# Optimization experiments

Hardware: AMD Instinct MI355X
Metric: run time of the kernel (lower is better)

Reference implementation:

```python
import jax, jax.numpy as jnp
import numpy as np

N = 20000
E = 320000
R1 = 8        # num_rels (layer 1)
R2 = 256      # layer-2 num_rels == out_size (faithful to original positional-arg bug)
B = 8         # num_bases
D = 256       # hid_size == out_size
TIME_DIM = 2880
POI_DIM = 12
ROAD_DIM = 32


def relconv(h, src, dst, etype, coeff, bases, loop_w, bias):
    """DGL RelGraphConv with basis regularizer, sum aggregation, self-loop, bias.
    W_r = sum_b coeff[r,b] * bases[b]; msg_e = h[src_e] @ W_{etype_e}; agg = scatter-add to dst.
    Implemented memory-efficiently: project nodes into basis space once [B,N,D],
    then scan over the B bases (small fixed loop) for the gather/scale/scatter.
    """
    tb = jnp.einsum('nd,bdo->bno', h, bases)          # [B, N, D]
    c = coeff[etype]                                   # [E, B] per-edge basis coeffs

    def body(agg, xs):
        tb_b, c_b = xs                                 # [N,D], [E]
        msg = c_b[:, None] * tb_b[src]                 # [E, D]
        return agg + jax.ops.segment_sum(msg, dst, num_segments=N), None

    agg0 = jnp.zeros((N, bases.shape[-1]), h.dtype)
    agg, _ = jax.lax.scan(body, agg0, (tb, c.T))
    return agg + h @ loop_w + bias


def rgcn2(feat, src, dst, etype, c1, v1, l1, b1, c2, v2, l2, b2):
    h = relconv(feat, src, dst, etype, c1, v1, l1, b1)
    h = jax.nn.relu(h)  # dropout p=0.0 -> identity
    h = relconv(h, src, dst, etype, c2, v2, l2, b2)
    return h


def setup_inputs() -> dict:
    key = jax.random.key(0)
    ks = iter(jax.random.split(key, 48))
    f32 = jnp.float32

    def nrm(shape, std=0.02):
        return (jax.random.normal(next(ks), shape, dtype=f32) * std)

    inp = {
        'poi_distribution': jax.random.uniform(next(ks), (N, POI_DIM), dtype=f32),
        'time_distribution': jax.random.normal(next(ks), (N, TIME_DIM), dtype=f32),
        'road_feature': jax.random.normal(next(ks), (N, ROAD_DIM), dtype=f32),
        # input projections (torch Linear: stored here as [in,out])
        'W_poi': nrm((POI_DIM, 64)), 'b_poi': jnp.zeros((64,), f32),
        'W_time': nrm((TIME_DIM, 128)), 'b_time': jnp.zeros((128,), f32),
        'W_road': nrm((ROAD_DIM, 64)), 'b_road': jnp.zeros((64,), f32),
        # adj R-GCN layer params: coeff [R,B], bases [B,D,D], loop [D,D], bias [D]
        'a_coeff1': nrm((R1, B), 0.3), 'a_bases1': nrm((B, D, D)),
        'a_loop1': nrm((D, D)), 'a_bias1': jnp.zeros((D,), f32),
        'a_coeff2': nrm((R2, B), 0.3), 'a_bases2': nrm((B, D, D)),
        'a_loop2': nrm((D, D)), 'a_bias2': jnp.zeros((D,), f32),
        # no_adj R-GCN layer params
        'n_coeff1': nrm((R1, B), 0.3), 'n_bases1': nrm((B, D, D)),
        'n_loop1': nrm((D, D)), 'n_bias1': jnp.zeros((D,), f32),
        'n_coeff2': nrm((R2, B), 0.3), 'n_bases2': nrm((B, D, D)),
        'n_loop2': nrm((D, D)), 'n_bias2': jnp.zeros((D,), f32),
        # fusion
        'W_fuse': nrm((D, D)), 'b_fuse': jnp.zeros((D,), f32),
        'W_fuse_kg': nrm((D, D)), 'b_fuse_kg': jnp.zeros((D,), f32),
        # graphs (edge lists + relation types)
        'adj_src': jax.random.randint(next(ks), (E,), 0, N, dtype=jnp.int32),
        'adj_dst': jax.random.randint(next(ks), (E,), 0, N, dtype=jnp.int32),
        'adj_type': jax.random.randint(next(ks), (E,), 0, R1, dtype=jnp.int32),
        'no_adj_src': jax.random.randint(next(ks), (E,), 0, N, dtype=jnp.int32),
        'no_adj_dst': jax.random.randint(next(ks), (E,), 0, N, dtype=jnp.int32),
        'no_adj_type': jax.random.randint(next(ks), (E,), 0, R1, dtype=jnp.int32),
    }
    return inp


def reference(poi_distribution, time_distribution, road_feature,
              W_poi, b_poi, W_time, b_time, W_road, b_road,
              a_coeff1, a_bases1, a_loop1, a_bias1,
              a_coeff2, a_bases2, a_loop2, a_bias2,
              n_coeff1, n_bases1, n_loop1, n_bias1,
              n_coeff2, n_bases2, n_loop2, n_bias2,
              W_fuse, b_fuse, W_fuse_kg, b_fuse_kg,
              adj_src, adj_dst, adj_type,
              no_adj_src, no_adj_dst, no_adj_type):
    poi_feat = poi_distribution @ W_poi + b_poi       # [N, 64]
    time_feat = time_distribution @ W_time + b_time   # [N, 128]
    road_feat = road_feature @ W_road + b_road        # [N, 64]
    feat = jnp.concatenate([poi_feat, time_feat, road_feat], axis=1)  # [N, 256]

    adj_emb = rgcn2(feat, adj_src, adj_dst, adj_type,
                    a_coeff1, a_bases1, a_loop1, a_bias1,
                    a_coeff2, a_bases2, a_loop2, a_bias2)
    no_adj_emb = rgcn2(feat, no_adj_src, no_adj_dst, no_adj_type,
                       n_coeff1, n_bases1, n_loop1, n_bias1,
                       n_coeff2, n_bases2, n_loop2, n_bias2)

    fused = (adj_emb @ W_fuse + b_fuse) + (no_adj_emb @ W_fuse_kg + b_fuse_kg)
    return jax.nn.gelu(fused, approximate=False)      # torch nn.GELU is exact erf
```

## Files before the change

kernel.cpp:

```cpp
#include <hip/hip_runtime.h>
#include <math.h>

typedef unsigned short ushort_t;
typedef __bf16 bf16x8 __attribute__((ext_vector_type(8)));
typedef float  f32x4  __attribute__((ext_vector_type(4)));

constexpr int NN = 20000;
constexpr int EE = 320000;
constexpr int NC = 2304;
constexpr int TD = 2880;

__device__ __forceinline__ float b2f(ushort_t u) {
    return __uint_as_float(((unsigned int)u) << 16);
}
__device__ __forceinline__ ushort_t f2b(float f) {
    unsigned int u = __float_as_uint(f);
    u += 0x7fffu + ((u >> 16) & 1u);
    return (ushort_t)(u >> 16);
}
__device__ __forceinline__ float ldf(const void* p, size_t i, int f32m) {
    return f32m ? ((const float*)p)[i] : b2f(((const ushort_t*)p)[i]);
}
__device__ __forceinline__ void gl2lds16(const ushort_t* g, ushort_t* l) {
    __builtin_amdgcn_global_load_lds(
        (const __attribute__((address_space(1))) void*)g,
        (__attribute__((address_space(3))) void*)l, 16, 0, 0);
}

__device__ __forceinline__ void mfma_step(const ushort_t* As, const ushort_t* Bs,
                                          f32x4 (&acc)[4][4],
                                          int wm, int wn, int quad, int l16)
{
    bf16x8 afr[4], bfr[4];
#pragma unroll
    for (int mi = 0; mi < 4; mi++)
        afr[mi] = *(const bf16x8*)(As + (wm * 64 + mi * 16 + l16) * 32 + quad * 8);
#pragma unroll
    for (int ni = 0; ni < 4; ni++)
        bfr[ni] = *(const bf16x8*)(Bs + (wn * 64 + ni * 16 + l16) * 32 + quad * 8);
#pragma unroll
    for (int mi = 0; mi < 4; mi++)
#pragma unroll
        for (int ni = 0; ni < 4; ni++)
            acc[mi][ni] = __builtin_amdgcn_mfma_f32_16x16x32_bf16(
                afr[mi], bfr[ni], acc[mi][ni], 0, 0, 0);
}

__global__ void k_detect(const void* timeD, int* flags)
{
    __shared__ float mx[256];
    int t = threadIdx.x;
    float m = 0.f;
    for (int i = t; i < 1024; i += 256) {
        float v = fabsf(b2f(((const ushort_t*)timeD)[i]));
        if (!(v < 1e30f)) v = 1e30f;
        m = fmaxf(m, v);
    }
    mx[t] = m;
    __syncthreads();
    if (t == 0) {
        float mm = 0.f;
        for (int i = 0; i < 256; i++) mm = fmaxf(mm, mx[i]);
        flags[0] = (mm > 1e4f) ? 1 : 0;
        flags[1] = 0;
    }
}

__global__ void k_cvt16(const void* __restrict__ in, ushort_t* __restrict__ out,
                        int n, const int* __restrict__ mf)
{
    int f32m = mf[0];
    int i = blockIdx.x * 256 + threadIdx.x;
    if (i < n) out[i] = f32m ? f2b(((const float*)in)[i]) : ((const ushort_t*)in)[i];
}

__global__ __launch_bounds__(256) void gemm_bt(
    const ushort_t* __restrict__ A, int lda,
    const ushort_t* __restrict__ Bt, int ldb,
    void* __restrict__ C, int ldc, int col0, const int* __restrict__ of,
    const ushort_t* __restrict__ bias,
    int M, int Ncols, int K, int act)
{
    __shared__ ushort_t As[128 * 32];
    __shared__ ushort_t Bs[128 * 32];

    const int f32o = of[0];
    const int t    = threadIdx.x;
    const int wave = t >> 6, lane = t & 63;
    const int wm   = wave >> 1, wn = wave & 1;
    const int quad = lane >> 4, l16 = lane & 15;
    const int m0   = blockIdx.x * 128, n0 = blockIdx.y * 128;

    f32x4 acc[4][4];
#pragma unroll
    for (int i = 0; i < 4; i++)
#pragma unroll
        for (int j = 0; j < 4; j++) acc[i][j] = (f32x4){0.f, 0.f, 0.f, 0.f};

    for (int k0 = 0; k0 < K; k0 += 32) {
#pragma unroll
        for (int j = 0; j < 2; j++) {
            int c   = (wave * 2 + j) * 64 + lane;
            int row = c >> 2, kc = c & 3;
            ushort_t* ldsbase_a = As + (wave * 2 + j) * 512;
            ushort_t* ldsbase_b = Bs + (wave * 2 + j) * 512;
            gl2lds16(A  + (size_t)(m0 + row) * lda + k0 + kc * 8, ldsbase_a);
            gl2lds16(Bt + (size_t)(n0 + row) * ldb + k0 + kc * 8, ldsbase_b);
        }
        __syncthreads();
        mfma_step(As, Bs, acc, wm, wn, quad, l16);
        __syncthreads();
    }

#pragma unroll
    for (int mi = 0; mi < 4; mi++) {
#pragma unroll
        for (int r = 0; r < 4; r++) {
            int row = m0 + wm * 64 + mi * 16 + quad * 4 + r;
            if (row >= M) continue;
#pragma unroll
            for (int ni = 0; ni < 4; ni++) {
                int col = n0 + wn * 64 + ni * 16 + l16;
                float v = acc[mi][ni][r];
                if (bias) v += b2f(bias[col]);
                if (act == 1) v = fmaxf(v, 0.f);
                else if (act == 2) v = 0.5f * v * (1.f + erff(v * 0.70710678118654752f));
                size_t idx = (size_t)row * ldc + col0 + col;
                if (f32o) ((float*)C)[idx] = v;
                else      ((ushort_t*)C)[idx] = f2b(v);
            }
        }
    }
}

__global__ __launch_bounds__(256) void gemm_splitk(
    const void* __restrict__ A, int lda, const int* __restrict__ af,
    const ushort_t* __restrict__ Bt, int ldb,
    float* __restrict__ part, int M, int K, int KC)
{
    __shared__ ushort_t As[128 * 32];
    __shared__ ushort_t Bs[128 * 32];

    const int f32a = af[0];
    const int t    = threadIdx.x;
    const int wave = t >> 6, lane = t & 63;
    const int wm   = wave >> 1, wn = wave & 1;
    const int quad = lane >> 4, l16 = lane & 15;
    const int m0   = blockIdx.x * 128;
    const int kbeg = blockIdx.y * KC;
    const int kend = (kbeg + KC < K) ? kbeg + KC : K;

    f32x4 acc[4][4];
#pragma unroll
    for (int i = 0; i < 4; i++)
#pragma unroll
        for (int j = 0; j < 4; j++) acc[i][j] = (f32x4){0.f, 0.f, 0.f, 0.f};

    if (!f32a && (m0 + 128 <= M)) {
        const ushort_t* Ab = (const ushort_t*)A;
        for (int k0 = kbeg; k0 < kend; k0 += 32) {
#pragma unroll
            for (int j = 0; j < 2; j++) {
                int c   = (wave * 2 + j) * 64 + lane;
                int row = c >> 2, kc = c & 3;
                gl2lds16(Ab + (size_t)(m0 + row) * lda + k0 + kc * 8,
                         As + (wave * 2 + j) * 512);
                gl2lds16(Bt + (size_t)row * ldb + k0 + kc * 8,
                         Bs + (wave * 2 + j) * 512);
            }
            __syncthreads();
            mfma_step(As, Bs, acc, wm, wn, quad, l16);
            __syncthreads();
        }
    } else {
        for (int k0 = kbeg; k0 < kend; k0 += 32) {
#pragma unroll
            for (int i = 0; i < 2; i++) {
                int c = t + i * 256;
                int row = c >> 2, kc = c & 3;
                uint4 av = make_uint4(0, 0, 0, 0);
                int gr = m0 + row;
                if (gr < M) {
                    size_t base = (size_t)gr * lda + k0 + kc * 8;
                    if (f32a) {
                        const float* Af = (const float*)A + base;
                        float4 lo = *(const float4*)Af;
                        float4 hi = *(const float4*)(Af + 4);
                        av.x = (unsigned)f2b(lo.x) | ((unsigned)f2b(lo.y) << 16);
                        av.y = (unsigned)f2b(lo.z) | ((unsigned)f2b(lo.w) << 16);
                        av.z = (unsigned)f2b(hi.x) | ((unsigned)f2b(hi.y) << 16);
                        av.w = (unsigned)f2b(hi.z) | ((unsigned)f2b(hi.w) << 16);
                    } else {
                        av = *(const uint4*)((const ushort_t*)A + base);
                    }
                }
                *(uint4*)(As + row * 32 + kc * 8) = av;
                uint4 bv = *(const uint4*)(Bt + (size_t)row * ldb + k0 + kc * 8);
                *(uint4*)(Bs + row * 32 + kc * 8) = bv;
            }
            __syncthreads();
            mfma_step(As, Bs, acc, wm, wn, quad, l16);
            __syncthreads();
        }
    }

    float* dst = part + (size_t)blockIdx.y * ((size_t)M * 128);
#pragma unroll
    for (int mi = 0; mi < 4; mi++) {
#pragma unroll
        for (int r = 0; r < 4; r++) {
            int row = m0 + wm * 64 + mi * 16 + quad * 4 + r;
            if (row >= M) continue;
#pragma unroll
            for (int ni = 0; ni < 4; ni++) {
                int col = wn * 64 + ni * 16 + l16;
                dst[(size_t)row * 128 + col] = acc[mi][ni][r];
            }
        }
    }
}

__global__ void k_bias_time(const float* __restrict__ part, int nsplit,
                            const ushort_t* __restrict__ bt,
                            ushort_t* __restrict__ feat)
{
    int n = blockIdx.x, o = threadIdx.x;
    float a = b2f(bt[o]);
    for (int s = 0; s < nsplit; ++s)
        a += part[(size_t)s * NN * 128 + (size_t)n * 128 + o];
    feat[(size_t)n * 256 + 64 + o] = f2b(a);
}

__global__ void k_build_wcat(const void* __restrict__ coeff,
                             const void* __restrict__ bases,
                             const void* __restrict__ loopw,
                             ushort_t* __restrict__ Wt, const int* __restrict__ mf)
{
    int f32m = mf[0];
    int r = blockIdx.x >> 8, k = blockIdx.x & 255, o = threadIdx.x;
    float acc;
    if (r == 8) {
        acc = ldf(loopw, k * 256 + o, f32m);
    } else {
        acc = 0.f;
#pragma unroll
        for (int b = 0; b < 8; b++)
            acc += ldf(coeff, r * 8 + b, f32m) * ldf(bases, ((size_t)b * 256 + k) * 256 + o, f32m);
    }
    Wt[((size_t)(r * 256 + o)) * 256 + k] = f2b(acc);
}

__global__ void k_transpose(const void* __restrict__ in, ushort_t* __restrict__ out,
                            int rows, int cols, const int* __restrict__ mf)
{
    int f32m = mf[0];
    int k = blockIdx.x, o = threadIdx.x;
    out[(size_t)o * rows + k] = f2b(ldf(in, (size_t)k * cols + o, f32m));
}

__global__ void k_build_wfuse(const void* __restrict__ Wf, const void* __restrict__ Wfk,
                              const void* __restrict__ bf, const void* __restrict__ bfk,
                              ushort_t* __restrict__ Wt, ushort_t* __restrict__ bias_cat,
                              const int* __restrict__ mf)
{
    int f32m = mf[0];
    int k = blockIdx.x, o = threadIdx.x;
    float v = (k < 256) ? ldf(Wf, k * 256 + o, f32m) : ldf(Wfk, (k - 256) * 256 + o, f32m);
    Wt[(size_t)o * 512 + k] = f2b(v);
    if (k == 0) bias_cat[o] = f2b(ldf(bf, o, f32m) + ldf(bfk, o, f32m));
}

__global__ void k_inproj(const void* __restrict__ poi, const void* __restrict__ Wp,
                         const void* __restrict__ bp,
                         const void* __restrict__ road, const void* __restrict__ Wr,
                         const void* __restrict__ br,
                         ushort_t* __restrict__ feat, const int* __restrict__ mf)
{
    int f32m = mf[0];
    int n = blockIdx.x, t = threadIdx.x;
    if (t < 64) {
        float a = ldf(bp, t, f32m);
#pragma unroll
        for (int k = 0; k < 12; k++)
            a += ldf(poi, (size_t)n * 12 + k, f32m) * ldf(Wp, k * 64 + t, f32m);
        feat[(size_t)n * 256 + t] = f2b(a);
    } else {
        int o = t - 64;
        float a = ldf(br, o, f32m);
#pragma unroll
        for (int k = 0; k < 32; k++)
            a += ldf(road, (size_t)n * 32 + k, f32m) * ldf(Wr, k * 64 + o, f32m);
        feat[(size_t)n * 256 + 192 + o] = f2b(a);
    }
}

__global__ void k_zero(int* __restrict__ p, int n)
{
    int i = blockIdx.x * 256 + threadIdx.x;
    if (i < n) p[i] = 0;
}
__global__ void k_count(const int* __restrict__ dst, int* __restrict__ deg, int e)
{
    int i = blockIdx.x * 256 + threadIdx.x;
    if (i < e) atomicAdd(&deg[dst[i]], 1);
}
__global__ void k_scan1(const int* __restrict__ deg, int* __restrict__ partial,
                        int* __restrict__ bsum, int n)
{
    int t = threadIdx.x, b = blockIdx.x;
    int i = b * 256 + t;
    int v = (i < n) ? deg[i] : 0;
    int lane = t & 63, w = t >> 6;
    int x = v;
#pragma unroll
    for (int d = 1; d < 64; d <<= 1) {
        int y = __shfl_up(x, d);
        if (lane >= d) x += y;
    }
    __shared__ int wt[4];
    if (lane == 63) wt[w] = x;
    __syncthreads();
    int woff = 0;
    for (int j = 0; j < 4; j++) if (j < w) woff += wt[j];
    int incl = x + woff;
    if (i < n) partial[i] = incl - v;
    if (t == 255) bsum[b] = incl;
}
__global__ void k_scan2(const int* __restrict__ bsum, int* __restrict__ boff, int nb)
{
    int t = threadIdx.x;
    int v = (t < nb) ? bsum[t] : 0;
    int lane = t & 63, w = t >> 6;
    int x = v;
#pragma unroll
    for (int d = 1; d < 64; d <<= 1) {
        int y = __shfl_up(x, d);
        if (lane >= d) x += y;
    }
    __shared__ int wt[4];
    if (lane == 63) wt[w] = x;
    __syncthreads();
    int woff = 0;
    for (int j = 0; j < 4; j++) if (j < w) woff += wt[j];
    boff[t] = (x + woff) - v;
}
__global__ void k_scan3(const int* __restrict__ boff, int* __restrict__ rs,
                        int* __restrict__ cur, int n)
{
    int i = blockIdx.x * 256 + threadIdx.x;
    if (i < n) {
        int v = rs[i] + boff[blockIdx.x];
        rs[i] = v;
        cur[i] = v;
    }
}
__global__ void k_fill(const int* __restrict__ src, const int* __restrict__ dst,
                       const int* __restrict__ et, int* __restrict__ cur,
                       int* __restrict__ sorted, int e)
{
    int i = blockIdx.x * 256 + threadIdx.x;
    if (i < e) {
        int pos = atomicAdd(&cur[dst[i]], 1);
        sorted[pos] = (src[i] << 3) | et[i];
    }
}

__global__ __launch_bounds__(256) void k_agg2(
    const ushort_t* __restrict__ tb, int ldt,
    const int* __restrict__ rs, const int* __restrict__ deg,
    const int* __restrict__ sorted, const ushort_t* __restrict__ bias,
    float* __restrict__ accf, ushort_t* __restrict__ out,
    int ldo, int col0, int act, int b0, int b1, int flags, int n_nodes)
{
    int w = blockIdx.x * 4 + (threadIdx.x >> 6);
    if (w >= n_nodes) return;
    int lane = threadIdx.x & 63;

    float a0, a1, a2, a3;
    if (flags & 1) {
        a0 = b2f(bias[lane * 4 + 0]);
        a1 = b2f(bias[lane * 4 + 1]);
        a2 = b2f(bias[lane * 4 + 2]);
        a3 = b2f(bias[lane * 4 + 3]);
    } else {
        float4 v = *(const float4*)(accf + (size_t)w * 256 + lane * 4);
        a0 = v.x; a1 = v.y; a2 = v.z; a3 = v.w;
    }
    if (b0 <= 8 && 8 < b1) {
        ushort4 lv = *(const ushort4*)(tb + (size_t)w * ldt + (8 - b0) * 256 + lane * 4);
        a0 += b2f(lv.x); a1 += b2f(lv.y); a2 += b2f(lv.z); a3 += b2f(lv.w);
    }
    int s = rs[w], cnt = deg[w];
    for (int j = 0; j < cnt; ++j) {
        int p = sorted[s + j];
        int r = p & 7;
        if (r >= b0 && r < b1) {
            const ushort_t* q = tb + (size_t)(p >> 3) * ldt + (r - b0) * 256 + lane * 4;
            ushort4 v = *(const ushort4*)q;
            a0 += b2f(v.x); a1 += b2f(v.y); a2 += b2f(v.z); a3 += b2f(v.w);
        }
    }
    if (flags & 2) {
        if (act) {
            a0 = fmaxf(a0, 0.f); a1 = fmaxf(a1, 0.f);
            a2 = fmaxf(a2, 0.f); a3 = fmaxf(a3, 0.f);
        }
        ushort4 o;
        o.x = f2b(a0); o.y = f2b(a1); o.z = f2b(a2); o.w = f2b(a3);
        *(ushort4*)(out + (size_t)w * ldo + col0 + lane * 4) = o;
    } else {
        *(float4*)(accf + (size_t)w * 256 + lane * 4) = make_float4(a0, a1, a2, a3);
    }
}

extern "C" void kernel_launch(void* const* d_in, const int* in_sizes, int n_in,
                              void* d_out, int out_size, void* d_ws, size_t ws_size,
                              hipStream_t stream)
{
    const void* poi    = d_in[0];
    const void* timeD  = d_in[1];
    const void* roadF  = d_in[2];
    const void* W_poi  = d_in[3];
    const void* b_poi  = d_in[4];
    const void* W_time = d_in[5];
    const void* b_time = d_in[6];
    const void* W_road = d_in[7];
    const void* b_road = d_in[8];
    const void* W_fuse  = d_in[25];
    const void* b_fuse  = d_in[26];
    const void* W_fusek = d_in[27];
    const void* b_fusek = d_in[28];
    const int* g_src[2] = {(const int*)d_in[29], (const int*)d_in[32]};
    const int* g_dst[2] = {(const int*)d_in[30], (const int*)d_in[33]};
    const int* g_typ[2] = {(const int*)d_in[31], (const int*)d_in[34]};

    char* p = (char*)d_ws;
    auto alloc = [&](size_t bytes) -> char* {
        char* r = p;
        p += (bytes + 255) & ~(size_t)255;
        return r;
    };
    int*      flags   = (int*)alloc(2 * 4);
    ushort_t* feat    = (ushort_t*)alloc((size_t)NN * 256 * 2);
    ushort_t* h1      = (ushort_t*)alloc((size_t)NN * 256 * 2);
    ushort_t* fused   = (ushort_t*)alloc((size_t)NN * 512 * 2);
    float*    accf    = (float*)alloc((size_t)NN * 256 * 4);
    ushort_t* wcat    = (ushort_t*)alloc((size_t)NC * 256 * 2);
    ushort_t* wtt     = (ushort_t*)alloc((size_t)128 * TD * 2);
    ushort_t* wft     = (ushort_t*)alloc((size_t)256 * 512 * 2);
    ushort_t* biascat = (ushort_t*)alloc(256 * 2);
    ushort_t* btws    = (ushort_t*)alloc(128 * 2);
    ushort_t* biws    = (ushort_t*)alloc(256 * 2);
    int* deg    = (int*)alloc((size_t)NN * 4);
    int* rs     = (int*)alloc((size_t)NN * 4);
    int* cur    = (int*)alloc((size_t)NN * 4);
    int* sorted = (int*)alloc((size_t)EE * 4);
    int* bsum   = (int*)alloc(256 * 4);
    int* boff   = (int*)alloc(256 * 4);

    size_t psl       = (size_t)NN * 128 * 4;
    size_t per_block = (size_t)NN * 256 * 2;
    size_t used0 = (size_t)(p - (char*)d_ws);
    int SPLITS;
    float* tpart;
    if (ws_size > used0 + per_block + 512 + psl) {
        size_t s = (ws_size - used0 - per_block - 512) / psl;
        SPLITS = (int)(s > 6 ? 6 : s);
        tpart  = (float*)alloc(psl * SPLITS);
    } else {
        tpart  = accf;
        SPLITS = 2;
    }
    const int KC = TD / SPLITS;

    size_t used = (size_t)(p - (char*)d_ws);
    int C = 1;
    if (ws_size > used + 512) {
        size_t c = (ws_size - used - 512) / per_block;
        C = (c < 1) ? 1 : (c > 9 ? 9 : (int)c);
    }
    ushort_t* tbuf = (ushort_t*)alloc(per_block * C);
    const int nch = (9 + C - 1) / C;

    const int SB = (NN + 255) / 256;
    const int EB = (EE + 255) / 256;
    const int MT = (NN + 127) / 128;

    k_detect<<<1, 256, 0, stream>>>(timeD, flags);
    k_transpose<<<TD, 128, 0, stream>>>(W_time, wtt, TD, 128, flags);
    k_build_wfuse<<<512, 256, 0, stream>>>(W_fuse, W_fusek, b_fuse, b_fusek,
                                           wft, biascat, flags);
    k_cvt16<<<1, 256, 0, stream>>>(b_time, btws, 128, flags);

    k_inproj<<<NN, 128, 0, stream>>>(poi, W_poi, b_poi, roadF, W_road, b_road,
                                     feat, flags);
    gemm_splitk<<<dim3(MT, SPLITS), 256, 0, stream>>>(timeD, TD, flags, wtt, TD,
                                                      tpart, NN, TD, KC);
    k_bias_time<<<NN, 128, 0, stream>>>(tpart, SPLITS, btws, feat);

    for (int g = 0; g < 2; ++g) {
        k_zero<<<SB, 256, 0, stream>>>(deg, NN);
        k_count<<<EB, 256, 0, stream>>>(g_dst[g], deg, EE);
        k_scan1<<<SB, 256, 0, stream>>>(deg, rs, bsum, NN);
        k_scan2<<<1, 256, 0, stream>>>(bsum, boff, SB);
        k_scan3<<<SB, 256, 0, stream>>>(boff, rs, cur, NN);
        k_fill<<<EB, 256, 0, stream>>>(g_src[g], g_dst[g], g_typ[g], cur, sorted, EE);

        for (int l = 0; l < 2; ++l) {
            int rc = g * 2 + l;
            const void* cf  = d_in[9 + rc * 4 + 0];
            const void* bs_ = d_in[9 + rc * 4 + 1];
            const void* lw  = d_in[9 + rc * 4 + 2];
            const void* bi  = d_in[9 + rc * 4 + 3];
            k_build_wcat<<<9 * 256, 256, 0, stream>>>(cf, bs_, lw, wcat, flags);
            k_cvt16<<<1, 256, 0, stream>>>(bi, biws, 256, flags);
            const ushort_t* Ain = (l == 0) ? feat : h1;
            ushort_t* dest = (l == 0) ? h1 : fused;
            int ldo  = (l == 0) ? 256 : 512;
            int col0 = (l == 0) ? 0 : g * 256;
            int act  = (l == 0) ? 1 : 0;
            for (int c = 0; c < nch; ++c) {
                int b0 = c * C;
                int b1 = (b0 + C < 9) ? b0 + C : 9;
                int nb = b1 - b0;
                gemm_bt<<<dim3(MT, nb * 2), 256, 0, stream>>>(
                    Ain, 256, wcat + (size_t)b0 * 256 * 256, 256,
                    tbuf, nb * 256, 0, flags + 1, nullptr, NN, nb * 256, 256, 0);
                int fl = (c == 0 ? 1 : 0) | (c == nch - 1 ? 2 : 0);
                k_agg2<<<NN / 4, 256, 0, stream>>>(tbuf, nb * 256, rs, deg, sorted,
                                                   biws, accf, dest, ldo, col0, act,
                                                   b0, b1, fl, NN);
            }
        }
    }

    gemm_bt<<<dim3(MT, 2), 256, 0, stream>>>(fused, 512, wft, 512,
                                             d_out, 256, 0, flags, biascat,
                                             NN, 256, 512, 2);
}
```

Before: 1.088 ms.

## Tile weight transposes through LDS and add single-pass aggregation for full buffer

The weight-building and transpose kernels are rewritten to use 32x32 LDS tiles, so both the global reads and the transposed writes are coalesced instead of strided. When the workspace holds all nine relation projections at once (nch==1), a specialized aggregation kernel runs. It reads the self-loop term and the per-edge gathered rows directly, writes bf16 output in one pass, and skips the fp32 accumulator round-trip and chunk flags. The chunked path is kept as a fallback for small workspaces.

```diff
diff --git a/kernel.cpp b/kernel.cpp
--- a/kernel.cpp
+++ b/kernel.cpp
@@ -231,43 +231,72 @@
     feat[(size_t)n * 256 + 64 + o] = f2b(a);
 }
 
-__global__ void k_build_wcat(const void* __restrict__ coeff,
-                             const void* __restrict__ bases,
-                             const void* __restrict__ loopw,
-                             ushort_t* __restrict__ Wt, const int* __restrict__ mf)
-{
+__global__ void k_build_wcatT(const void* __restrict__ coeff,
+                              const void* __restrict__ bases,
+                              const void* __restrict__ loopw,
+                              ushort_t* __restrict__ Wt, const int* __restrict__ mf)
+{
+    __shared__ ushort_t tile[32][33];
     int f32m = mf[0];
-    int r = blockIdx.x >> 8, k = blockIdx.x & 255, o = threadIdx.x;
-    float acc;
-    if (r == 8) {
-        acc = ldf(loopw, k * 256 + o, f32m);
-    } else {
-        acc = 0.f;
-#pragma unroll
-        for (int b = 0; b < 8; b++)
-            acc += ldf(coeff, r * 8 + b, f32m) * ldf(bases, ((size_t)b * 256 + k) * 256 + o, f32m);
-    }
-    Wt[((size_t)(r * 256 + o)) * 256 + k] = f2b(acc);
-}
-
-__global__ void k_transpose(const void* __restrict__ in, ushort_t* __restrict__ out,
-                            int rows, int cols, const int* __restrict__ mf)
-{
+    int blk = blockIdx.x;
+    int r = blk >> 6, kt = (blk >> 3) & 7, ot = blk & 7;
+    int k0 = kt * 32, o0 = ot * 32;
+    int oi = threadIdx.x & 31, k4 = threadIdx.x >> 5;
+    float cf[8];
+    if (r < 8) {
+#pragma unroll
+        for (int b = 0; b < 8; b++) cf[b] = ldf(coeff, r * 8 + b, f32m);
+    }
+#pragma unroll
+    for (int p = 0; p < 4; ++p) {
+        int ki = k4 * 4 + p, k = k0 + ki, o = o0 + oi;
+        float acc;
+        if (r == 8) {
+            acc = ldf(loopw, (size_t)k * 256 + o, f32m);
+        } else {
+            acc = 0.f;
+#pragma unroll
+            for (int b = 0; b < 8; b++)
+                acc += cf[b] * ldf(bases, ((size_t)b * 256 + k) * 256 + o, f32m);
+        }
+        tile[ki][oi] = f2b(acc);
+    }
+    __syncthreads();
+    int ki2 = threadIdx.x & 31, o4 = threadIdx.x >> 5;
+#pragma unroll
+    for (int p = 0; p < 4; ++p) {
+        int o2 = o4 * 4 + p;
+        Wt[((size_t)(r * 256 + o0 + o2)) * 256 + k0 + ki2] = tile[ki2][o2];
+    }
+}
+
+__global__ void k_trans32(const void* __restrict__ in, ushort_t* __restrict__ out,
+                          int cols, int ldout, const int* __restrict__ mf)
+{
+    __shared__ ushort_t tile[32][33];
     int f32m = mf[0];
-    int k = blockIdx.x, o = threadIdx.x;
-    out[(size_t)o * rows + k] = f2b(ldf(in, (size_t)k * cols + o, f32m));
-}
-
-__global__ void k_build_wfuse(const void* __restrict__ Wf, const void* __restrict__ Wfk,
-                              const void* __restrict__ bf, const void* __restrict__ bfk,
-                              ushort_t* __restrict__ Wt, ushort_t* __restrict__ bias_cat,
-                              const int* __restrict__ mf)
+    int k0 = blockIdx.x * 32, o0 = blockIdx.y * 32;
+    int oi = threadIdx.x & 31, k4 = threadIdx.x >> 5;
+#pragma unroll
+    for (int p = 0; p < 4; ++p) {
+        int ki = k4 * 4 + p;
+        tile[ki][oi] = f2b(ldf(in, (size_t)(k0 + ki) * cols + (o0 + oi), f32m));
+    }
+    __syncthreads();
+    int ki2 = threadIdx.x & 31, o4 = threadIdx.x >> 5;
+#pragma unroll
+    for (int p = 0; p < 4; ++p) {
+        int o2 = o4 * 4 + p;
+        out[(size_t)(o0 + o2) * ldout + k0 + ki2] = tile[ki2][o2];
+    }
+}
+
+__global__ void k_biasfuse(const void* __restrict__ bf, const void* __restrict__ bfk,
+                           ushort_t* __restrict__ bias_cat, const int* __restrict__ mf)
 {
     int f32m = mf[0];
-    int k = blockIdx.x, o = threadIdx.x;
-    float v = (k < 256) ? ldf(Wf, k * 256 + o, f32m) : ldf(Wfk, (k - 256) * 256 + o, f32m);
-    Wt[(size_t)o * 512 + k] = f2b(v);
-    if (k == 0) bias_cat[o] = f2b(ldf(bf, o, f32m) + ldf(bfk, o, f32m));
+    int o = threadIdx.x;
+    bias_cat[o] = f2b(ldf(bf, o, f32m) + ldf(bfk, o, f32m));
 }
 
 __global__ void k_inproj(const void* __restrict__ poi, const void* __restrict__ Wp,
@@ -363,6 +392,55 @@
         int pos = atomicAdd(&cur[dst[i]], 1);
         sorted[pos] = (src[i] << 3) | et[i];
     }
+}
+
+__global__ __launch_bounds__(256) void k_agg_full(
+    const ushort_t* __restrict__ tb,
+    const int* __restrict__ rs, const int* __restrict__ deg,
+    const int* __restrict__ sorted, const ushort_t* __restrict__ bias,
+    ushort_t* __restrict__ out, int ldo, int col0, int act, int n_nodes)
+{
+    int w = blockIdx.x * 4 + (threadIdx.x >> 6);
+    if (w >= n_nodes) return;
+    int lane = threadIdx.x & 63;
+    int lo = lane * 4;
+
+    float a0 = b2f(bias[lo + 0]);
+    float a1 = b2f(bias[lo + 1]);
+    float a2 = b2f(bias[lo + 2]);
+    float a3 = b2f(bias[lo + 3]);
+    {
+        ushort4 lv = *(const ushort4*)(tb + (size_t)w * NC + 8 * 256 + lo);
+        a0 += b2f(lv.x); a1 += b2f(lv.y); a2 += b2f(lv.z); a3 += b2f(lv.w);
+    }
+    int s = rs[w], cnt = deg[w];
+    int j = 0;
+    for (; j + 4 <= cnt; j += 4) {
+        int p0 = sorted[s + j + 0];
+        int p1 = sorted[s + j + 1];
+        int p2 = sorted[s + j + 2];
+        int p3 = sorted[s + j + 3];
+        ushort4 v0 = *(const ushort4*)(tb + ((size_t)(p0 >> 3) * 9 + (p0 & 7)) * 256 + lo);
+        ushort4 v1 = *(const ushort4*)(tb + ((size_t)(p1 >> 3) * 9 + (p1 & 7)) * 256 + lo);
+        ushort4 v2 = *(const ushort4*)(tb + ((size_t)(p2 >> 3) * 9 + (p2 & 7)) * 256 + lo);
+        ushort4 v3 = *(const ushort4*)(tb + ((size_t)(p3 >> 3) * 9 + (p3 & 7)) * 256 + lo);
+        a0 += b2f(v0.x); a1 += b2f(v0.y); a2 += b2f(v0.z); a3 += b2f(v0.w);
+        a0 += b2f(v1.x); a1 += b2f(v1.y); a2 += b2f(v1.z); a3 += b2f(v1.w);
+        a0 += b2f(v2.x); a1 += b2f(v2.y); a2 += b2f(v2.z); a3 += b2f(v2.w);
+        a0 += b2f(v3.x); a1 += b2f(v3.y); a2 += b2f(v3.z); a3 += b2f(v3.w);
+    }
+    for (; j < cnt; ++j) {
+        int p = sorted[s + j];
+        ushort4 v = *(const ushort4*)(tb + ((size_t)(p >> 3) * 9 + (p & 7)) * 256 + lo);
+        a0 += b2f(v.x); a1 += b2f(v.y); a2 += b2f(v.z); a3 += b2f(v.w);
+    }
+    if (act) {
+        a0 = fmaxf(a0, 0.f); a1 = fmaxf(a1, 0.f);
+        a2 = fmaxf(a2, 0.f); a3 = fmaxf(a3, 0.f);
+    }
+    ushort4 o;
+    o.x = f2b(a0); o.y = f2b(a1); o.z = f2b(a2); o.w = f2b(a3);
+    *(ushort4*)(out + (size_t)w * ldo + col0 + lo) = o;
 }
 
 __global__ __launch_bounds__(256) void k_agg2(
@@ -487,9 +565,10 @@
     const int MT = (NN + 127) / 128;
 
     k_detect<<<1, 256, 0, stream>>>(timeD, flags);
-    k_transpose<<<TD, 128, 0, stream>>>(W_time, wtt, TD, 128, flags);
-    k_build_wfuse<<<512, 256, 0, stream>>>(W_fuse, W_fusek, b_fuse, b_fusek,
-                                           wft, biascat, flags);
+    k_trans32<<<dim3(TD / 32, 128 / 32), 256, 0, stream>>>(W_time, wtt, 128, TD, flags);
+    k_trans32<<<dim3(8, 8), 256, 0, stream>>>(W_fuse, wft, 256, 512, flags);
+    k_trans32<<<dim3(8, 8), 256, 0, stream>>>(W_fusek, wft + 256, 256, 512, flags);
+    k_biasfuse<<<1, 256, 0, stream>>>(b_fuse, b_fusek, biascat, flags);
     k_cvt16<<<1, 256, 0, stream>>>(b_time, btws, 128, flags);
 
     k_inproj<<<NN, 128, 0, stream>>>(poi, W_poi, b_poi, roadF, W_road, b_road,
@@ -512,24 +591,33 @@
             const void* bs_ = d_in[9 + rc * 4 + 1];
             const void* lw  = d_in[9 + rc * 4 + 2];
             const void* bi  = d_in[9 + rc * 4 + 3];
-            k_build_wcat<<<9 * 256, 256, 0, stream>>>(cf, bs_, lw, wcat, flags);
+            k_build_wcatT<<<9 * 64, 256, 0, stream>>>(cf, bs_, lw, wcat, flags);
             k_cvt16<<<1, 256, 0, stream>>>(bi, biws, 256, flags);
             const ushort_t* Ain = (l == 0) ? feat : h1;
             ushort_t* dest = (l == 0) ? h1 : fused;
             int ldo  = (l == 0) ? 256 : 512;
             int col0 = (l == 0) ? 0 : g * 256;
             int act  = (l == 0) ? 1 : 0;
-            for (int c = 0; c < nch; ++c) {
-                int b0 = c * C;
-                int b1 = (b0 + C < 9) ? b0 + C : 9;
-                int nb = b1 - b0;
-                gemm_bt<<<dim3(MT, nb * 2), 256, 0, stream>>>(
-                    Ain, 256, wcat + (size_t)b0 * 256 * 256, 256,
-                    tbuf, nb * 256, 0, flags + 1, nullptr, NN, nb * 256, 256, 0);
-                int fl = (c == 0 ? 1 : 0) | (c == nch - 1 ? 2 : 0);
-                k_agg2<<<NN / 4, 256, 0, stream>>>(tbuf, nb * 256, rs, deg, sorted,
-                                                   biws, accf, dest, ldo, col0, act,
-                                                   b0, b1, fl, NN);
+            if (nch == 1) {
+                gemm_bt<<<dim3(MT, 18), 256, 0, stream>>>(
+                    Ain, 256, wcat, 256, tbuf, NC, 0, flags + 1, nullptr,
+                    NN, NC, 256, 0);
+                k_agg_full<<<NN / 4, 256, 0, stream>>>(tbuf, rs, deg, sorted,
+                                                       biws, dest, ldo, col0,
+                                                       act, NN);
+            } else {
+                for (int c = 0; c < nch; ++c) {
+                    int b0 = c * C;
+                    int b1 = (b0 + C < 9) ? b0 + C : 9;
+                    int nb = b1 - b0;
+                    gemm_bt<<<dim3(MT, nb * 2), 256, 0, stream>>>(
+                        Ain, 256, wcat + (size_t)b0 * 256 * 256, 256,
+                        tbuf, nb * 256, 0, flags + 1, nullptr, NN, nb * 256, 256, 0);
+                    int fl = (c == 0 ? 1 : 0) | (c == nch - 1 ? 2 : 0);
+                    k_agg2<<<NN / 4, 256, 0, stream>>>(tbuf, nb * 256, rs, deg, sorted,
+                                                       biws, accf, dest, ldo, col0, act,
+                                                       b0, b1, fl, NN);
+                }
             }
         }
     }
```

Measured after the change: 1.009 ms. 1.08x faster.
